# Performance work log

Hardware: AMD Instinct MI355X
Metric: run time of the kernel (lower is better)

The kernel has to match this reference:

```python
import jax, jax.numpy as jnp
import numpy as np

NUM_HEADS = 2
LN_EPS = 1e-5
NEG_MASK = -1e9


def setup_inputs() -> dict:
    key = jax.random.key(0)
    ks = jax.random.split(key, 8)
    B, C, T, N = 8, 64, 32, 400
    H, D = NUM_HEADS, C // NUM_HEADS
    s = 1.0 / np.sqrt(C)
    return {
        "x": jax.random.normal(ks[0], (B, C, T, N), dtype=jnp.float32),
        "Wq": jax.random.normal(ks[1], (C, C), dtype=jnp.float32) * s,
        "Wk": jax.random.normal(ks[2], (C, C), dtype=jnp.float32) * s,
        "Wv": jax.random.normal(ks[3], (C, C), dtype=jnp.float32) * s,
        "a_src": jax.random.normal(ks[4], (H, D), dtype=jnp.float32) * 0.1,
        "a_dst": jax.random.normal(ks[5], (H, D), dtype=jnp.float32) * 0.1,
        "ln_gamma": jnp.ones((C,), dtype=jnp.float32),
        "ln_beta": jnp.zeros((C,), dtype=jnp.float32),
        "gso": jax.random.randint(ks[6], (N, N), 0, 2, dtype=jnp.int32),
    }


def reference(x, Wq, Wk, Wv, a_src, a_dst, ln_gamma, ln_beta, gso):
    B, C, T, N = x.shape
    H = NUM_HEADS
    D = C // H
    # (B,C,T,N) -> (B*T, N, C)
    xr = jnp.transpose(x, (0, 2, 3, 1)).reshape(B * T, N, C)
    # torch Linear: y = x @ W.T; then split heads -> (BT, N, H, D)
    Q = (xr @ Wq.T).reshape(B * T, N, H, D)
    K = (xr @ Wk.T).reshape(B * T, N, H, D)
    V = (xr @ Wv.T).reshape(B * T, N, H, D)
    # GAT additive scores per head
    s_src = jnp.einsum("bnhd,hd->bnh", Q, a_src)  # (BT, N, H)
    s_dst = jnp.einsum("bnhd,hd->bnh", K, a_dst)  # (BT, N, H)
    scores = s_src[:, :, None, :] + s_dst[:, None, :, :]  # (BT, i, j, H)
    scores = jax.nn.leaky_relu(scores, negative_slope=0.2)
    mask = jnp.where(gso == 0, jnp.float32(NEG_MASK), 0.0)  # (N, N)
    scores = scores + mask[None, :, :, None]
    attn = jax.nn.softmax(scores, axis=2)  # softmax over dst j; dropout = identity (eval)
    out = jnp.einsum("bijh,bjhd->bihd", attn, V).reshape(B * T, N, C)
    # LayerNorm over channel dim
    mu = jnp.mean(out, axis=-1, keepdims=True)
    var = jnp.var(out, axis=-1, keepdims=True)
    out = (out - mu) * jax.lax.rsqrt(var + LN_EPS) * ln_gamma + ln_beta
    # (BT, N, C) -> (B, C, T, N)
    return jnp.transpose(out.reshape(B, T, N, C), (0, 3, 1, 2))
```

## Files before the change

### kernel.cpp

```cpp
#include <hip/hip_runtime.h>
#include <hip/hip_bf16.h>

typedef __attribute__((ext_vector_type(8))) short bf16x8;
typedef __attribute__((ext_vector_type(4))) float f32x4;
typedef __attribute__((ext_vector_type(2))) float f32x2;
typedef __attribute__((ext_vector_type(4))) int i32x4;
typedef __attribute__((ext_vector_type(4))) unsigned int u32x4;
typedef __attribute__((ext_vector_type(2))) unsigned int u32x2;

#define B_   8
#define C_   64
#define T_   32
#define N_   400
#define BT_  256
#define NKT_ 13
#define CN_  12800
#define VROW 424
#define WROW 72
#define OBW  65
#define L2E_ 1.4426950408889634f
#define SH6_ (-8.656170245333780f)

#if __has_builtin(__builtin_amdgcn_exp2f)
#define EXP2F(x) __builtin_amdgcn_exp2f(x)
#else
#define EXP2F(x) __expf((x) * 0.6931471805599453f)
#endif

__global__ __launch_bounds__(256) void gat_prep(
    const int* __restrict__ gso, unsigned int* __restrict__ mb)
{
  int idx = blockIdx.x*256 + threadIdx.x;
  if (idx < N_*16) {
    int i = idx >> 4, kw = idx & 15;
    unsigned int bits = 0;
    if (kw < 13) {
      int j0 = kw * 32;
      #pragma unroll
      for (int bb = 0; bb < 32; ++bb) {
        int j = j0 + bb;
        if (j < N_ && gso[i*N_ + j] != 0) bits |= (1u << bb);
      }
    }
    mb[idx] = bits;
  }
}

__global__ __launch_bounds__(1024) void gat_fused(
    const float* __restrict__ x, const float* __restrict__ Wq,
    const float* __restrict__ Wk, const float* __restrict__ Wv,
    const float* __restrict__ a_src, const float* __restrict__ a_dst,
    const float* __restrict__ gamma, const float* __restrict__ beta,
    const unsigned int* __restrict__ mb, float* __restrict__ out)
{
  __shared__ __align__(16) __hip_bfloat16 Vt[64][VROW];
  __shared__ __align__(16) __hip_bfloat16 wvb[80][WROW];
  __shared__ __align__(16) float e1d_s[2][416];
  __shared__ __align__(16) float e2d_s[2][416];
  __shared__ __align__(16) float si_s[2][400];
  __shared__ __align__(16) float ob[128][OBW];
  __shared__ __align__(16) unsigned int lut_s[16][2];
  __shared__ float g_s[64], b_s[64];

  const int tid = threadIdx.x;
  const int bt = blockIdx.x;
  const int b = bt >> 5, t = bt & 31;
  const int lane = tid & 63, wave = tid >> 6;
  const int col = lane & 15, quad = lane >> 4;

  const float* xbase = x + ((size_t)b*C_*T_ + t)*N_;
  float xf0[2][8];
  {
    const int n0 = wave*16;
    #pragma unroll
    for (int kt = 0; kt < 2; ++kt) {
      const float* xc = xbase + (size_t)(kt*32 + quad*8)*CN_ + n0 + col;
      #pragma unroll
      for (int j = 0; j < 8; ++j) xf0[kt][j] = xc[(size_t)j*CN_];
    }
  }

  #pragma unroll
  for (int it = 0; it < 4; ++it) {
    int idx = it*1024 + tid;
    int o = idx >> 6, c = idx & 63;
    wvb[o][c] = __float2bfloat16(Wv[o*C_ + c]);
  }
  if (tid < 256) {
    int ww = tid >> 6, c = tid & 63, h = ww >> 1;
    const float* W = (ww & 1) ? Wk : Wq;
    const float* a = (ww & 1) ? a_dst : a_src;
    float s = 0.f;
    #pragma unroll
    for (int d = 0; d < 32; ++d) s += W[(h*32 + d)*C_ + c] * a[h*32 + d];
    wvb[64 + ww][c] = __float2bfloat16(s * L2E_);
  } else if (tid < 320) {
    g_s[tid - 256] = gamma[tid - 256];
  } else if (tid < 384) {
    b_s[tid - 320] = beta[tid - 320];
  } else if (tid < 448) {
    int tt = tid - 384;
    int h = (tt >> 4) & 1, cc = 400 + (tt & 15);
    if (tt < 32) e1d_s[h][cc] = 0.f; else e2d_s[h][cc] = 0.f;
  } else if (tid < 464) {
    int n = tid - 448;
    lut_s[n][0] = ((n & 1) ? 0x0000FFFFu : 0u) | ((n & 2) ? 0xFFFF0000u : 0u);
    lut_s[n][1] = ((n & 4) ? 0x0000FFFFu : 0u) | ((n & 8) ? 0xFFFF0000u : 0u);
  }
  for (int idx = tid; idx < 12*WROW; idx += 1024)
    wvb[68 + idx/WROW][idx % WROW] = __float2bfloat16(0.f);
  for (int idx = tid; idx < 64*24; idx += 1024)
    Vt[idx/24][400 + idx%24] = __float2bfloat16(0.f);
  __syncthreads();

  {
    auto proj_tile = [&](int n0, const float xf[2][8]) {
      bf16x8 bfrag[2];
      #pragma unroll
      for (int kt = 0; kt < 2; ++kt) {
        union { short s[8]; bf16x8 v; } pk;
        #pragma unroll
        for (int j = 0; j < 8; ++j) {
          union { __hip_bfloat16 h; short s; } cv;
          cv.h = __float2bfloat16(xf[kt][j]);
          pk.s[j] = cv.s;
        }
        bfrag[kt] = pk.v;
      }
      #pragma unroll
      for (int ot = 0; ot < 5; ++ot) {
        f32x4 acc = {0.f, 0.f, 0.f, 0.f};
        #pragma unroll
        for (int kt = 0; kt < 2; ++kt) {
          bf16x8 afr = *(const bf16x8*)&wvb[ot*16 + col][kt*32 + quad*8];
          acc = __builtin_amdgcn_mfma_f32_16x16x32_bf16(afr, bfrag[kt], acc, 0, 0, 0);
        }
        if (ot < 4) {
          #pragma unroll
          for (int r = 0; r < 4; ++r)
            Vt[ot*16 + quad*4 + r][n0 + col] = __float2bfloat16(acc[r]);
        } else if (quad == 0) {
          #pragma unroll
          for (int r = 0; r < 4; ++r) {
            int h = r >> 1;
            if (r & 1) {
              e1d_s[h][n0 + col] = EXP2F(acc[r] + SH6_);
              e2d_s[h][n0 + col] = EXP2F(fmaf(0.2f, acc[r], SH6_));
            } else {
              si_s[h][n0 + col] = acc[r];
            }
          }
        }
      }
    };

    proj_tile(wave*16, xf0);
    if (wave < 9) {
      float xf1[2][8];
      const int n0 = (wave + 16)*16;
      #pragma unroll
      for (int kt = 0; kt < 2; ++kt) {
        const float* xc = xbase + (size_t)(kt*32 + quad*8)*CN_ + n0 + col;
        #pragma unroll
        for (int j = 0; j < 8; ++j) xf1[kt][j] = xc[(size_t)j*CN_];
      }
      proj_tile(n0, xf1);
    }
  }
  __syncthreads();

  const int hh = wave & 1, itile = wave >> 1;
  const int rowA = col;
  const unsigned int qsh = quad * 8;

  bf16x8 ones;
  #pragma unroll
  for (int k = 0; k < 8; ++k) ones[k] = (short)0x3F80;

  for (int r0 = 0; r0 < N_; r0 += 128) {
    const int ibase = r0 + itile*16;
    if (ibase < N_) {
      const int irow = ibase + rowA;
      const float si1 = si_s[hh][irow];
      const float E1i = EXP2F(si1 + SH6_);
      const float E2i = EXP2F(fmaf(0.2f, si1, SH6_));
      const u32x4* mp = (const u32x4*)(mb + irow*16);
      u32x4 mw0 = mp[0], mw1 = mp[1], mw2 = mp[2];
      unsigned int mw12 = mb[irow*16 + 12];
      const float* e1p = e1d_s[hh] + quad*8;
      const float* e2p = e2d_s[hh] + quad*8;
      const __hip_bfloat16* v0p = &Vt[hh*32 + rowA][quad*8];
      const __hip_bfloat16* v1p = v0p + 16*VROW;
      const f32x2 e1g = {E1i, E1i};
      const f32x2 e2g = {E2i, E2i};

      f32x4 d0 = {0,0,0,0}, d1 = {0,0,0,0}, d2 = {0,0,0,0};
      #pragma unroll
      for (int kt = 0; kt < NKT_; ++kt) {
        unsigned int mword = (kt < 4) ? mw0[kt] : (kt < 8) ? mw1[kt-4]
                           : (kt < 12) ? mw2[kt-8] : mw12;
        unsigned int mbyte = (mword >> qsh) & 0xffu;
        u32x2 mlo = *(const u32x2*)&lut_s[mbyte & 15u][0];
        u32x2 mhi = *(const u32x2*)&lut_s[mbyte >> 4][0];
        union { f32x4 v4[2]; f32x2 v2[4]; } u1, u2;
        u1.v4[0] = *(const f32x4*)(e1p + kt*32);
        u1.v4[1] = *(const f32x4*)(e1p + kt*32 + 4);
        u2.v4[0] = *(const f32x4*)(e2p + kt*32);
        u2.v4[1] = *(const f32x4*)(e2p + kt*32 + 4);
        bf16x8 vb0 = *(const bf16x8*)(v0p + kt*32);
        bf16x8 vb1 = *(const bf16x8*)(v1p + kt*32);
        u32x2 w[4];
        #pragma unroll
        for (int q2 = 0; q2 < 4; ++q2) {
          f32x2 a = e1g * u1.v2[q2];
          f32x2 c = e2g * u2.v2[q2];
          f32x2 m = {fmaxf(a.x, c.x), fmaxf(a.y, c.y)};
          union { f32x2 f; u32x2 u; } cvt; cvt.f = m;
          w[q2] = cvt.u;
        }
        union { i32x4 i; bf16x8 v; } af;
        af.i.x = (int)(__builtin_amdgcn_perm(w[0].y, w[0].x, 0x07060302u) & mlo.x);
        af.i.y = (int)(__builtin_amdgcn_perm(w[1].y, w[1].x, 0x07060302u) & mlo.y);
        af.i.z = (int)(__builtin_amdgcn_perm(w[2].y, w[2].x, 0x07060302u) & mhi.x);
        af.i.w = (int)(__builtin_amdgcn_perm(w[3].y, w[3].x, 0x07060302u) & mhi.y);
        d0 = __builtin_amdgcn_mfma_f32_16x16x32_bf16(af.v, vb0, d0, 0, 0, 0);
        d1 = __builtin_amdgcn_mfma_f32_16x16x32_bf16(af.v, vb1, d1, 0, 0, 0);
        d2 = __builtin_amdgcn_mfma_f32_16x16x32_bf16(af.v, ones, d2, 0, 0, 0);
      }
      #pragma unroll
      for (int r = 0; r < 4; ++r) {
        float li = 1.0f / d2[r];
        int rl = itile*16 + quad*4 + r;
        ob[rl][hh*32 + rowA]      = d0[r] * li;
        ob[rl][hh*32 + 16 + rowA] = d1[r] * li;
      }
    }
    __syncthreads();

    {
      int rl = tid >> 3, cgi = tid & 7;
      int n = r0 + rl;
      if (n < N_) {
        float u[8]; float s = 0.f;
        #pragma unroll
        for (int k = 0; k < 8; ++k) { u[k] = ob[rl][cgi*8 + k]; s += u[k]; }
        s += __shfl_xor(s,1); s += __shfl_xor(s,2); s += __shfl_xor(s,4);
        float mu = s * (1.f/64.f);
        float q = 0.f;
        #pragma unroll
        for (int k = 0; k < 8; ++k) { float dv = u[k]-mu; q = fmaf(dv,dv,q); }
        q += __shfl_xor(q,1); q += __shfl_xor(q,2); q += __shfl_xor(q,4);
        float rstd = rsqrtf(q*(1.f/64.f) + 1e-5f);
        #pragma unroll
        for (int k = 0; k < 8; ++k)
          ob[rl][cgi*8 + k] = (u[k]-mu)*rstd*g_s[cgi*8 + k] + b_s[cgi*8 + k];
      }
    }
    __syncthreads();

    #pragma unroll
    for (int it = 0; it < 8; ++it) {
      int idx = it*1024 + tid;
      int c = idx >> 7, nn = idx & 127;
      int n = r0 + nn;
      if (n < N_) out[((size_t)(b*C_ + c)*T_ + t)*N_ + n] = ob[nn][c];
    }
    __syncthreads();
  }
}

extern "C" void kernel_launch(void* const* d_in, const int* in_sizes, int n_in,
                              void* d_out, int out_size, void* d_ws, size_t ws_size,
                              hipStream_t stream) {
  (void)in_sizes; (void)n_in; (void)out_size; (void)ws_size;
  const float* x     = (const float*)d_in[0];
  const float* Wq    = (const float*)d_in[1];
  const float* Wk    = (const float*)d_in[2];
  const float* Wv    = (const float*)d_in[3];
  const float* a_src = (const float*)d_in[4];
  const float* a_dst = (const float*)d_in[5];
  const float* gamma = (const float*)d_in[6];
  const float* beta  = (const float*)d_in[7];
  const int*   gso   = (const int*)d_in[8];
  float* out = (float*)d_out;

  unsigned int* mbp = (unsigned int*)d_ws;

  gat_prep<<<26, 256, 0, stream>>>(gso, mbp);
  gat_fused<<<BT_, 1024, 0, stream>>>(x, Wq, Wk, Wv, a_src, a_dst,
                                      gamma, beta, mbp, out);
}
```

Before: 117.3 us.

## Process two row tiles per wave to share loads and cut passes

```diff
diff --git a/kernel.cpp b/kernel.cpp
--- a/kernel.cpp
+++ b/kernel.cpp
@@ -58,7 +58,7 @@
   __shared__ __align__(16) float e1d_s[2][416];
   __shared__ __align__(16) float e2d_s[2][416];
   __shared__ __align__(16) float si_s[2][400];
-  __shared__ __align__(16) float ob[128][OBW];
+  __shared__ __align__(16) float ob[256][OBW];
   __shared__ __align__(16) unsigned int lut_s[16][2];
   __shared__ float g_s[64], b_s[64];
 
@@ -169,7 +169,7 @@
   }
   __syncthreads();
 
-  const int hh = wave & 1, itile = wave >> 1;
+  const int hh = wave & 1, slot = wave >> 1;
   const int rowA = col;
   const unsigned int qsh = quad * 8;
 
@@ -177,43 +177,52 @@
   #pragma unroll
   for (int k = 0; k < 8; ++k) ones[k] = (short)0x3F80;
 
-  for (int r0 = 0; r0 < N_; r0 += 128) {
-    const int ibase = r0 + itile*16;
-    if (ibase < N_) {
-      const int irow = ibase + rowA;
-      const float si1 = si_s[hh][irow];
-      const float E1i = EXP2F(si1 + SH6_);
-      const float E2i = EXP2F(fmaf(0.2f, si1, SH6_));
-      const u32x4* mp = (const u32x4*)(mb + irow*16);
-      u32x4 mw0 = mp[0], mw1 = mp[1], mw2 = mp[2];
-      unsigned int mw12 = mb[irow*16 + 12];
-      const float* e1p = e1d_s[hh] + quad*8;
-      const float* e2p = e2d_s[hh] + quad*8;
-      const __hip_bfloat16* v0p = &Vt[hh*32 + rowA][quad*8];
-      const __hip_bfloat16* v1p = v0p + 16*VROW;
-      const f32x2 e1g = {E1i, E1i};
-      const f32x2 e2g = {E2i, E2i};
-
-      f32x4 d0 = {0,0,0,0}, d1 = {0,0,0,0}, d2 = {0,0,0,0};
-      #pragma unroll
-      for (int kt = 0; kt < NKT_; ++kt) {
-        unsigned int mword = (kt < 4) ? mw0[kt] : (kt < 8) ? mw1[kt-4]
-                           : (kt < 12) ? mw2[kt-8] : mw12;
+  const float* e1p = e1d_s[hh] + quad*8;
+  const float* e2p = e2d_s[hh] + quad*8;
+  const __hip_bfloat16* v0p = &Vt[hh*32 + rowA][quad*8];
+  const __hip_bfloat16* v1p = v0p + 16*VROW;
+
+  auto sweep = [&](int r0, int itA, int itB, bool aB) {
+    const int irA = itA*16 + rowA;
+    const int irB = itB*16 + rowA;
+    const float siA = si_s[hh][irA];
+    const f32x2 e1A = {EXP2F(siA + SH6_), EXP2F(siA + SH6_)};
+    const f32x2 e2A = {EXP2F(fmaf(0.2f, siA, SH6_)), EXP2F(fmaf(0.2f, siA, SH6_))};
+    const float siB = si_s[hh][irB];
+    const f32x2 e1B = {EXP2F(siB + SH6_), EXP2F(siB + SH6_)};
+    const f32x2 e2B = {EXP2F(fmaf(0.2f, siB, SH6_)), EXP2F(fmaf(0.2f, siB, SH6_))};
+
+    const u32x4* mpA = (const u32x4*)(mb + irA*16);
+    u32x4 mA0 = mpA[0], mA1 = mpA[1], mA2 = mpA[2];
+    unsigned int mA12 = mb[irA*16 + 12];
+    const u32x4* mpB = (const u32x4*)(mb + irB*16);
+    u32x4 mB0 = mpB[0], mB1 = mpB[1], mB2 = mpB[2];
+    unsigned int mB12 = mb[irB*16 + 12];
+
+    f32x4 d0A={0,0,0,0}, d1A={0,0,0,0}, d2A={0,0,0,0};
+    f32x4 d0B={0,0,0,0}, d1B={0,0,0,0}, d2B={0,0,0,0};
+
+    #pragma unroll
+    for (int kt = 0; kt < NKT_; ++kt) {
+      union { f32x4 v4[2]; f32x2 v2[4]; } u1, u2;
+      u1.v4[0] = *(const f32x4*)(e1p + kt*32);
+      u1.v4[1] = *(const f32x4*)(e1p + kt*32 + 4);
+      u2.v4[0] = *(const f32x4*)(e2p + kt*32);
+      u2.v4[1] = *(const f32x4*)(e2p + kt*32 + 4);
+      bf16x8 vb0 = *(const bf16x8*)(v0p + kt*32);
+      bf16x8 vb1 = *(const bf16x8*)(v1p + kt*32);
+
+      {
+        unsigned int mword = (kt < 4) ? mA0[kt] : (kt < 8) ? mA1[kt-4]
+                           : (kt < 12) ? mA2[kt-8] : mA12;
         unsigned int mbyte = (mword >> qsh) & 0xffu;
         u32x2 mlo = *(const u32x2*)&lut_s[mbyte & 15u][0];
         u32x2 mhi = *(const u32x2*)&lut_s[mbyte >> 4][0];
-        union { f32x4 v4[2]; f32x2 v2[4]; } u1, u2;
-        u1.v4[0] = *(const f32x4*)(e1p + kt*32);
-        u1.v4[1] = *(const f32x4*)(e1p + kt*32 + 4);
-        u2.v4[0] = *(const f32x4*)(e2p + kt*32);
-        u2.v4[1] = *(const f32x4*)(e2p + kt*32 + 4);
-        bf16x8 vb0 = *(const bf16x8*)(v0p + kt*32);
-        bf16x8 vb1 = *(const bf16x8*)(v1p + kt*32);
         u32x2 w[4];
         #pragma unroll
         for (int q2 = 0; q2 < 4; ++q2) {
-          f32x2 a = e1g * u1.v2[q2];
-          f32x2 c = e2g * u2.v2[q2];
+          f32x2 a = e1A * u1.v2[q2];
+          f32x2 c = e2A * u2.v2[q2];
           f32x2 m = {fmaxf(a.x, c.x), fmaxf(a.y, c.y)};
           union { f32x2 f; u32x2 u; } cvt; cvt.f = m;
           w[q2] = cvt.u;
@@ -223,24 +232,60 @@
         af.i.y = (int)(__builtin_amdgcn_perm(w[1].y, w[1].x, 0x07060302u) & mlo.y);
         af.i.z = (int)(__builtin_amdgcn_perm(w[2].y, w[2].x, 0x07060302u) & mhi.x);
         af.i.w = (int)(__builtin_amdgcn_perm(w[3].y, w[3].x, 0x07060302u) & mhi.y);
-        d0 = __builtin_amdgcn_mfma_f32_16x16x32_bf16(af.v, vb0, d0, 0, 0, 0);
-        d1 = __builtin_amdgcn_mfma_f32_16x16x32_bf16(af.v, vb1, d1, 0, 0, 0);
-        d2 = __builtin_amdgcn_mfma_f32_16x16x32_bf16(af.v, ones, d2, 0, 0, 0);
-      }
+        d0A = __builtin_amdgcn_mfma_f32_16x16x32_bf16(af.v, vb0, d0A, 0, 0, 0);
+        d1A = __builtin_amdgcn_mfma_f32_16x16x32_bf16(af.v, vb1, d1A, 0, 0, 0);
+        d2A = __builtin_amdgcn_mfma_f32_16x16x32_bf16(af.v, ones, d2A, 0, 0, 0);
+      }
+      if (aB) {
+        unsigned int mword = (kt < 4) ? mB0[kt] : (kt < 8) ? mB1[kt-4]
+                           : (kt < 12) ? mB2[kt-8] : mB12;
+        unsigned int mbyte = (mword >> qsh) & 0xffu;
+        u32x2 mlo = *(const u32x2*)&lut_s[mbyte & 15u][0];
+        u32x2 mhi = *(const u32x2*)&lut_s[mbyte >> 4][0];
+        u32x2 w[4];
+        #pragma unroll
+        for (int q2 = 0; q2 < 4; ++q2) {
+          f32x2 a = e1B * u1.v2[q2];
+          f32x2 c = e2B * u2.v2[q2];
+          f32x2 m = {fmaxf(a.x, c.x), fmaxf(a.y, c.y)};
+          union { f32x2 f; u32x2 u; } cvt; cvt.f = m;
+          w[q2] = cvt.u;
+        }
+        union { i32x4 i; bf16x8 v; } af;
+        af.i.x = (int)(__builtin_amdgcn_perm(w[0].y, w[0].x, 0x07060302u) & mlo.x);
+        af.i.y = (int)(__builtin_amdgcn_perm(w[1].y, w[1].x, 0x07060302u) & mlo.y);
+        af.i.z = (int)(__builtin_amdgcn_perm(w[2].y, w[2].x, 0x07060302u) & mhi.x);
+        af.i.w = (int)(__builtin_amdgcn_perm(w[3].y, w[3].x, 0x07060302u) & mhi.y);
+        d0B = __builtin_amdgcn_mfma_f32_16x16x32_bf16(af.v, vb0, d0B, 0, 0, 0);
+        d1B = __builtin_amdgcn_mfma_f32_16x16x32_bf16(af.v, vb1, d1B, 0, 0, 0);
+        d2B = __builtin_amdgcn_mfma_f32_16x16x32_bf16(af.v, ones, d2B, 0, 0, 0);
+      }
+    }
+
+    {
       #pragma unroll
       for (int r = 0; r < 4; ++r) {
-        float li = 1.0f / d2[r];
-        int rl = itile*16 + quad*4 + r;
-        ob[rl][hh*32 + rowA]      = d0[r] * li;
-        ob[rl][hh*32 + 16 + rowA] = d1[r] * li;
-      }
-    }
-    __syncthreads();
-
-    {
-      int rl = tid >> 3, cgi = tid & 7;
-      int n = r0 + rl;
-      if (n < N_) {
+        float li = 1.0f / d2A[r];
+        int rl = itA*16 - r0 + quad*4 + r;
+        ob[rl][hh*32 + rowA]      = d0A[r] * li;
+        ob[rl][hh*32 + 16 + rowA] = d1A[r] * li;
+      }
+    }
+    if (aB) {
+      #pragma unroll
+      for (int r = 0; r < 4; ++r) {
+        float li = 1.0f / d2B[r];
+        int rl = itB*16 - r0 + quad*4 + r;
+        ob[rl][hh*32 + rowA]      = d0B[r] * li;
+        ob[rl][hh*32 + 16 + rowA] = d1B[r] * li;
+      }
+    }
+  };
+
+  auto ln_store = [&](int r0, int rows) {
+    for (int rr = 0; rr < rows; rr += 128) {
+      int rl = rr + (tid >> 3), cgi = tid & 7;
+      if (rl < rows) {
         float u[8]; float s = 0.f;
         #pragma unroll
         for (int k = 0; k < 8; ++k) { u[k] = ob[rl][cgi*8 + k]; s += u[k]; }
@@ -257,16 +302,24 @@
       }
     }
     __syncthreads();
-
-    #pragma unroll
-    for (int it = 0; it < 8; ++it) {
-      int idx = it*1024 + tid;
-      int c = idx >> 7, nn = idx & 127;
-      int n = r0 + nn;
-      if (n < N_) out[((size_t)(b*C_ + c)*T_ + t)*N_ + n] = ob[nn][c];
-    }
-    __syncthreads();
-  }
+    for (int rr = 0; rr < rows; rr += 128) {
+      #pragma unroll
+      for (int it = 0; it < 8; ++it) {
+        int idx = it*1024 + tid;
+        int c = idx >> 7, nn = idx & 127;
+        int rl = rr + nn;
+        if (rl < rows) out[((size_t)(b*C_ + c)*T_ + t)*N_ + r0 + rl] = ob[rl][c];
+      }
+    }
+  };
+
+  sweep(0, slot, slot + 8, true);
+  __syncthreads();
+  ln_store(0, 256);
+  __syncthreads();
+  sweep(256, 16 + slot, 24, slot == 0);
+  __syncthreads();
+  ln_store(256, N_ - 256);
 }
 
 extern "C" void kernel_launch(void* const* d_in, const int* in_sizes, int n_in,
```

Result: no change. 116.6 us (-0.5%).

## Assign both heads per wave and fuse LayerNorm into attention epilogue via shuffles

Applied to the files above, without the earlier changes.

```diff
diff --git a/kernel.cpp b/kernel.cpp
--- a/kernel.cpp
+++ b/kernel.cpp
@@ -18,6 +18,7 @@
 #define VROW 424
 #define WROW 72
 #define OBW  65
+#define OBROWS 208
 #define L2E_ 1.4426950408889634f
 #define SH6_ (-8.656170245333780f)
 
@@ -58,7 +59,7 @@
   __shared__ __align__(16) float e1d_s[2][416];
   __shared__ __align__(16) float e2d_s[2][416];
   __shared__ __align__(16) float si_s[2][400];
-  __shared__ __align__(16) float ob[128][OBW];
+  __shared__ __align__(16) float ob[OBROWS][OBW];
   __shared__ __align__(16) unsigned int lut_s[16][2];
   __shared__ float g_s[64], b_s[64];
 
@@ -169,7 +170,6 @@
   }
   __syncthreads();
 
-  const int hh = wave & 1, itile = wave >> 1;
   const int rowA = col;
   const unsigned int qsh = quad * 8;
 
@@ -177,43 +177,61 @@
   #pragma unroll
   for (int k = 0; k < 8; ++k) ones[k] = (short)0x3F80;
 
-  for (int r0 = 0; r0 < N_; r0 += 128) {
-    const int ibase = r0 + itile*16;
-    if (ibase < N_) {
-      const int irow = ibase + rowA;
-      const float si1 = si_s[hh][irow];
-      const float E1i = EXP2F(si1 + SH6_);
-      const float E2i = EXP2F(fmaf(0.2f, si1, SH6_));
-      const u32x4* mp = (const u32x4*)(mb + irow*16);
-      u32x4 mw0 = mp[0], mw1 = mp[1], mw2 = mp[2];
-      unsigned int mw12 = mb[irow*16 + 12];
-      const float* e1p = e1d_s[hh] + quad*8;
-      const float* e2p = e2d_s[hh] + quad*8;
-      const __hip_bfloat16* v0p = &Vt[hh*32 + rowA][quad*8];
-      const __hip_bfloat16* v1p = v0p + 16*VROW;
-      const f32x2 e1g = {E1i, E1i};
-      const f32x2 e2g = {E2i, E2i};
-
-      f32x4 d0 = {0,0,0,0}, d1 = {0,0,0,0}, d2 = {0,0,0,0};
-      #pragma unroll
-      for (int kt = 0; kt < NKT_; ++kt) {
-        unsigned int mword = (kt < 4) ? mw0[kt] : (kt < 8) ? mw1[kt-4]
-                           : (kt < 12) ? mw2[kt-8] : mw12;
-        unsigned int mbyte = (mword >> qsh) & 0xffu;
-        u32x2 mlo = *(const u32x2*)&lut_s[mbyte & 15u][0];
-        u32x2 mhi = *(const u32x2*)&lut_s[mbyte >> 4][0];
+  float gr0 = g_s[col],      gr1 = g_s[16 + col],
+        gr2 = g_s[32 + col], gr3 = g_s[48 + col];
+  float br0 = b_s[col],      br1 = b_s[16 + col],
+        br2 = b_s[32 + col], br3 = b_s[48 + col];
+
+  const float* e1p0 = e1d_s[0] + quad*8;
+  const float* e2p0 = e2d_s[0] + quad*8;
+  const float* e1p1 = e1d_s[1] + quad*8;
+  const float* e2p1 = e2d_s[1] + quad*8;
+  const __hip_bfloat16* v00p = &Vt[rowA][quad*8];
+  const __hip_bfloat16* v01p = v00p + 16*VROW;
+  const __hip_bfloat16* v10p = &Vt[32 + rowA][quad*8];
+  const __hip_bfloat16* v11p = v10p + 16*VROW;
+
+  struct Res { f32x4 a00, a01, a10, a11, s0, s1; };
+
+  auto sweep = [&](int itile) -> Res {
+    const int irow = itile*16 + rowA;
+    const float si0 = si_s[0][irow];
+    const float si1 = si_s[1][irow];
+    const float E10s = EXP2F(si0 + SH6_), E20s = EXP2F(fmaf(0.2f, si0, SH6_));
+    const float E11s = EXP2F(si1 + SH6_), E21s = EXP2F(fmaf(0.2f, si1, SH6_));
+    const f32x2 e1A = {E10s, E10s}, e2A = {E20s, E20s};
+    const f32x2 e1B = {E11s, E11s}, e2B = {E21s, E21s};
+
+    const u32x4* mp = (const u32x4*)(mb + irow*16);
+    u32x4 mw0 = mp[0], mw1 = mp[1], mw2 = mp[2];
+    unsigned int mw12 = mb[irow*16 + 12];
+
+    Res R;
+    R.a00 = (f32x4){0,0,0,0}; R.a01 = (f32x4){0,0,0,0};
+    R.a10 = (f32x4){0,0,0,0}; R.a11 = (f32x4){0,0,0,0};
+    R.s0  = (f32x4){0,0,0,0}; R.s1  = (f32x4){0,0,0,0};
+
+    #pragma unroll
+    for (int kt = 0; kt < NKT_; ++kt) {
+      unsigned int mword = (kt < 4) ? mw0[kt] : (kt < 8) ? mw1[kt-4]
+                         : (kt < 12) ? mw2[kt-8] : mw12;
+      unsigned int mbyte = (mword >> qsh) & 0xffu;
+      u32x2 mlo = *(const u32x2*)&lut_s[mbyte & 15u][0];
+      u32x2 mhi = *(const u32x2*)&lut_s[mbyte >> 4][0];
+
+      {
         union { f32x4 v4[2]; f32x2 v2[4]; } u1, u2;
-        u1.v4[0] = *(const f32x4*)(e1p + kt*32);
-        u1.v4[1] = *(const f32x4*)(e1p + kt*32 + 4);
-        u2.v4[0] = *(const f32x4*)(e2p + kt*32);
-        u2.v4[1] = *(const f32x4*)(e2p + kt*32 + 4);
-        bf16x8 vb0 = *(const bf16x8*)(v0p + kt*32);
-        bf16x8 vb1 = *(const bf16x8*)(v1p + kt*32);
+        u1.v4[0] = *(const f32x4*)(e1p0 + kt*32);
+        u1.v4[1] = *(const f32x4*)(e1p0 + kt*32 + 4);
+        u2.v4[0] = *(const f32x4*)(e2p0 + kt*32);
+        u2.v4[1] = *(const f32x4*)(e2p0 + kt*32 + 4);
+        bf16x8 vb0 = *(const bf16x8*)(v00p + kt*32);
+        bf16x8 vb1 = *(const bf16x8*)(v01p + kt*32);
         u32x2 w[4];
         #pragma unroll
         for (int q2 = 0; q2 < 4; ++q2) {
-          f32x2 a = e1g * u1.v2[q2];
-          f32x2 c = e2g * u2.v2[q2];
+          f32x2 a = e1A * u1.v2[q2];
+          f32x2 c = e2A * u2.v2[q2];
           f32x2 m = {fmaxf(a.x, c.x), fmaxf(a.y, c.y)};
           union { f32x2 f; u32x2 u; } cvt; cvt.f = m;
           w[q2] = cvt.u;
@@ -223,50 +241,90 @@
         af.i.y = (int)(__builtin_amdgcn_perm(w[1].y, w[1].x, 0x07060302u) & mlo.y);
         af.i.z = (int)(__builtin_amdgcn_perm(w[2].y, w[2].x, 0x07060302u) & mhi.x);
         af.i.w = (int)(__builtin_amdgcn_perm(w[3].y, w[3].x, 0x07060302u) & mhi.y);
-        d0 = __builtin_amdgcn_mfma_f32_16x16x32_bf16(af.v, vb0, d0, 0, 0, 0);
-        d1 = __builtin_amdgcn_mfma_f32_16x16x32_bf16(af.v, vb1, d1, 0, 0, 0);
-        d2 = __builtin_amdgcn_mfma_f32_16x16x32_bf16(af.v, ones, d2, 0, 0, 0);
-      }
-      #pragma unroll
-      for (int r = 0; r < 4; ++r) {
-        float li = 1.0f / d2[r];
-        int rl = itile*16 + quad*4 + r;
-        ob[rl][hh*32 + rowA]      = d0[r] * li;
-        ob[rl][hh*32 + 16 + rowA] = d1[r] * li;
-      }
-    }
-    __syncthreads();
-
-    {
-      int rl = tid >> 3, cgi = tid & 7;
-      int n = r0 + rl;
-      if (n < N_) {
-        float u[8]; float s = 0.f;
-        #pragma unroll
-        for (int k = 0; k < 8; ++k) { u[k] = ob[rl][cgi*8 + k]; s += u[k]; }
-        s += __shfl_xor(s,1); s += __shfl_xor(s,2); s += __shfl_xor(s,4);
-        float mu = s * (1.f/64.f);
-        float q = 0.f;
-        #pragma unroll
-        for (int k = 0; k < 8; ++k) { float dv = u[k]-mu; q = fmaf(dv,dv,q); }
-        q += __shfl_xor(q,1); q += __shfl_xor(q,2); q += __shfl_xor(q,4);
-        float rstd = rsqrtf(q*(1.f/64.f) + 1e-5f);
-        #pragma unroll
-        for (int k = 0; k < 8; ++k)
-          ob[rl][cgi*8 + k] = (u[k]-mu)*rstd*g_s[cgi*8 + k] + b_s[cgi*8 + k];
-      }
-    }
-    __syncthreads();
-
+        R.a00 = __builtin_amdgcn_mfma_f32_16x16x32_bf16(af.v, vb0, R.a00, 0, 0, 0);
+        R.a01 = __builtin_amdgcn_mfma_f32_16x16x32_bf16(af.v, vb1, R.a01, 0, 0, 0);
+        R.s0  = __builtin_amdgcn_mfma_f32_16x16x32_bf16(af.v, ones, R.s0, 0, 0, 0);
+      }
+      {
+        union { f32x4 v4[2]; f32x2 v2[4]; } u1, u2;
+        u1.v4[0] = *(const f32x4*)(e1p1 + kt*32);
+        u1.v4[1] = *(const f32x4*)(e1p1 + kt*32 + 4);
+        u2.v4[0] = *(const f32x4*)(e2p1 + kt*32);
+        u2.v4[1] = *(const f32x4*)(e2p1 + kt*32 + 4);
+        bf16x8 vb0 = *(const bf16x8*)(v10p + kt*32);
+        bf16x8 vb1 = *(const bf16x8*)(v11p + kt*32);
+        u32x2 w[4];
+        #pragma unroll
+        for (int q2 = 0; q2 < 4; ++q2) {
+          f32x2 a = e1B * u1.v2[q2];
+          f32x2 c = e2B * u2.v2[q2];
+          f32x2 m = {fmaxf(a.x, c.x), fmaxf(a.y, c.y)};
+          union { f32x2 f; u32x2 u; } cvt; cvt.f = m;
+          w[q2] = cvt.u;
+        }
+        union { i32x4 i; bf16x8 v; } af;
+        af.i.x = (int)(__builtin_amdgcn_perm(w[0].y, w[0].x, 0x07060302u) & mlo.x);
+        af.i.y = (int)(__builtin_amdgcn_perm(w[1].y, w[1].x, 0x07060302u) & mlo.y);
+        af.i.z = (int)(__builtin_amdgcn_perm(w[2].y, w[2].x, 0x07060302u) & mhi.x);
+        af.i.w = (int)(__builtin_amdgcn_perm(w[3].y, w[3].x, 0x07060302u) & mhi.y);
+        R.a10 = __builtin_amdgcn_mfma_f32_16x16x32_bf16(af.v, vb0, R.a10, 0, 0, 0);
+        R.a11 = __builtin_amdgcn_mfma_f32_16x16x32_bf16(af.v, vb1, R.a11, 0, 0, 0);
+        R.s1  = __builtin_amdgcn_mfma_f32_16x16x32_bf16(af.v, ones, R.s1, 0, 0, 0);
+      }
+    }
+    return R;
+  };
+
+  auto write_ln = [&](const Res& R, int itile, int r0pass) {
     #pragma unroll
-    for (int it = 0; it < 8; ++it) {
-      int idx = it*1024 + tid;
-      int c = idx >> 7, nn = idx & 127;
-      int n = r0 + nn;
-      if (n < N_) out[((size_t)(b*C_ + c)*T_ + t)*N_ + n] = ob[nn][c];
-    }
-    __syncthreads();
-  }
+    for (int r = 0; r < 4; ++r) {
+      float li0 = 1.0f / R.s0[r];
+      float li1 = 1.0f / R.s1[r];
+      float v0 = R.a00[r] * li0;
+      float v1 = R.a01[r] * li0;
+      float v2 = R.a10[r] * li1;
+      float v3 = R.a11[r] * li1;
+      float s = v0 + v1 + v2 + v3;
+      s += __shfl_xor(s, 1); s += __shfl_xor(s, 2);
+      s += __shfl_xor(s, 4); s += __shfl_xor(s, 8);
+      float mu = s * (1.f/64.f);
+      float d0v = v0 - mu, d1v = v1 - mu, d2v = v2 - mu, d3v = v3 - mu;
+      float q = d0v*d0v; q = fmaf(d1v, d1v, q);
+      q = fmaf(d2v, d2v, q); q = fmaf(d3v, d3v, q);
+      q += __shfl_xor(q, 1); q += __shfl_xor(q, 2);
+      q += __shfl_xor(q, 4); q += __shfl_xor(q, 8);
+      float rstd = rsqrtf(q*(1.f/64.f) + 1e-5f);
+      int rl = itile*16 - r0pass + quad*4 + r;
+      ob[rl][     col] = d0v*rstd*gr0 + br0;
+      ob[rl][16 + col] = d1v*rstd*gr1 + br1;
+      ob[rl][32 + col] = d2v*rstd*gr2 + br2;
+      ob[rl][48 + col] = d3v*rstd*gr3 + br3;
+    }
+  };
+
+  auto store_rows = [&](int r0, int rows) {
+    for (int rr = 0; rr < rows; rr += 128) {
+      #pragma unroll
+      for (int it = 0; it < 8; ++it) {
+        int idx = it*1024 + tid;
+        int c = idx >> 7, nn = idx & 127;
+        int rl = rr + nn;
+        if (rl < rows)
+          out[((size_t)(b*C_ + c)*T_ + t)*N_ + r0 + rl] = ob[rl][c];
+      }
+    }
+  };
+
+  Res RA;
+  if (wave < 13) { RA = sweep(wave); write_ln(RA, wave, 0); }
+  __syncthreads();
+  store_rows(0, OBROWS);
+  Res RB;
+  if (wave < 12) RB = sweep(13 + wave);
+  __syncthreads();
+  if (wave < 12) write_ln(RB, 13 + wave, OBROWS);
+  __syncthreads();
+  store_rows(OBROWS, N_ - OBROWS);
 }
 
 extern "C" void kernel_launch(void* const* d_in, const int* in_sizes, int n_in,
```

Result: no change. 117.3 us (+0.0%).
